# Kernel tuning notes

Hardware: AMD Instinct MI355X
Metric: run time of the kernel (lower is better)

Reference implementation:

```python
import jax, jax.numpy as jnp
import numpy as np

N_NODES = 170000
N_EDGES = 1200000
IN_FEATS = 128
N_HIDDEN = 256
N_CLASSES = 40
BN_EPS = 1e-5


def setup_inputs() -> dict:
    key = jax.random.key(0)
    ks = jax.random.split(key, 12)
    feat = jax.random.normal(ks[0], (N_NODES, IN_FEATS), dtype=jnp.float32)
    src = jax.random.randint(ks[1], (N_EDGES,), 0, N_NODES, dtype=jnp.int32)
    dst = jax.random.randint(ks[2], (N_EDGES,), 0, N_NODES, dtype=jnp.int32)
    # GraphConv weights (glorot-ish scale) and last-layer bias
    W0 = jax.random.normal(ks[3], (IN_FEATS, N_HIDDEN), dtype=jnp.float32) * (1.0 / np.sqrt(IN_FEATS))
    W1 = jax.random.normal(ks[4], (N_HIDDEN, N_HIDDEN), dtype=jnp.float32) * (1.0 / np.sqrt(N_HIDDEN))
    W2 = jax.random.normal(ks[5], (N_HIDDEN, N_CLASSES), dtype=jnp.float32) * (1.0 / np.sqrt(N_HIDDEN))
    b2 = jnp.zeros((N_CLASSES,), dtype=jnp.float32)
    # BatchNorm affine params for the two hidden layers
    g0 = jnp.ones((N_HIDDEN,), dtype=jnp.float32)
    beta0 = jnp.zeros((N_HIDDEN,), dtype=jnp.float32)
    g1 = jnp.ones((N_HIDDEN,), dtype=jnp.float32)
    beta1 = jnp.zeros((N_HIDDEN,), dtype=jnp.float32)
    return {"feat": feat, "src": src, "dst": dst, "W0": W0, "W1": W1, "W2": W2,
            "b2": b2, "g0": g0, "beta0": beta0, "g1": g1, "beta1": beta1}


def _batchnorm(h, gamma, beta):
    mean = jnp.mean(h, axis=0)
    var = jnp.mean((h - mean) ** 2, axis=0)  # biased var, torch training-mode norm
    return (h - mean) * jax.lax.rsqrt(var + BN_EPS) * gamma + beta


def reference(feat, src, dst, W0, W1, W2, b2, g0, beta0, g1, beta1):
    n = feat.shape[0]
    ones_e = jnp.ones(src.shape, dtype=feat.dtype)
    deg_out = jnp.clip(jax.ops.segment_sum(ones_e, src, num_segments=n), 1.0)
    deg_in = jnp.clip(jax.ops.segment_sum(ones_e, dst, num_segments=n), 1.0)
    norm_src = deg_out ** -0.5  # [N]
    norm_dst = deg_in ** -0.5   # [N]

    def conv(h, W, bias=None):
        # GraphConv 'both': D_out^{-1/2} message, sum-aggregate, D_in^{-1/2}
        h = h @ W                              # project first (out <= in)
        msg = h[src] * norm_src[src][:, None]  # [E, out]
        agg = jax.ops.segment_sum(msg, dst, num_segments=n) * norm_dst[:, None]
        if bias is not None:
            agg = agg + bias
        return agg

    # dropout layers are identity in this deterministic (eval-style) reference
    h = conv(feat, W0)
    h = jax.nn.relu(_batchnorm(h, g0, beta0))
    h = conv(h, W1)
    h = jax.nn.relu(_batchnorm(h, g1, beta1))
    h = conv(h, W2, b2)
    return h
```

## Files before the change

kernel.cpp:

```cpp
#include <hip/hip_runtime.h>

#define NN 170000
#define NE 1200000
#define F_IN 128
#define F_HID 256
#define F_OUT 40
#define BN_EPS 1e-5f
#define SCAN_B ((NN + 255) / 256)
#define GB64 ((NN + 63) / 64)
#define STAT_ROWS GB64
#define STAT_CHUNK 32
#define STAT_NCH ((STAT_ROWS + STAT_CHUNK - 1) / STAT_CHUNK)

typedef __attribute__((ext_vector_type(8))) short short8;
typedef __attribute__((ext_vector_type(4))) float f32x4;
typedef __attribute__((ext_vector_type(4))) unsigned short us4;
typedef __attribute__((ext_vector_type(4))) unsigned int u32x4;

__device__ __forceinline__ float b2f(unsigned short u) {
    union { unsigned x; float f; } c; c.x = ((unsigned)u) << 16; return c.f;
}
__device__ __forceinline__ unsigned short f2b(float f) {
    union { float f; unsigned x; } c; c.f = f;
    unsigned r = (c.x + 0x7FFFu + ((c.x >> 16) & 1u)) >> 16;
    return (unsigned short)r;
}

__device__ __forceinline__ void agg_sum(const u32x4& v, float (&aa)[8]) {
    aa[0] += b2f((unsigned short)(v.x & 0xffffu)); aa[1] += b2f((unsigned short)(v.x >> 16));
    aa[2] += b2f((unsigned short)(v.y & 0xffffu)); aa[3] += b2f((unsigned short)(v.y >> 16));
    aa[4] += b2f((unsigned short)(v.z & 0xffffu)); aa[5] += b2f((unsigned short)(v.z >> 16));
    aa[6] += b2f((unsigned short)(v.w & 0xffffu)); aa[7] += b2f((unsigned short)(v.w >> 16));
}
__device__ __forceinline__ void agg_fuse(const u32x4& v, float ns,
        const f32x4& ca0, const f32x4& ca1, const f32x4& cb0, const f32x4& cb1, float (&aa)[8]) {
    aa[0] += fmaxf(fmaf(b2f((unsigned short)(v.x & 0xffffu)), ca0.x, cb0.x), 0.f) * ns;
    aa[1] += fmaxf(fmaf(b2f((unsigned short)(v.x >> 16)),     ca0.y, cb0.y), 0.f) * ns;
    aa[2] += fmaxf(fmaf(b2f((unsigned short)(v.y & 0xffffu)), ca0.z, cb0.z), 0.f) * ns;
    aa[3] += fmaxf(fmaf(b2f((unsigned short)(v.y >> 16)),     ca0.w, cb0.w), 0.f) * ns;
    aa[4] += fmaxf(fmaf(b2f((unsigned short)(v.z & 0xffffu)), ca1.x, cb1.x), 0.f) * ns;
    aa[5] += fmaxf(fmaf(b2f((unsigned short)(v.z >> 16)),     ca1.y, cb1.y), 0.f) * ns;
    aa[6] += fmaxf(fmaf(b2f((unsigned short)(v.w & 0xffffu)), ca1.z, cb1.z), 0.f) * ns;
    aa[7] += fmaxf(fmaf(b2f((unsigned short)(v.w >> 16)),     ca1.w, cb1.w), 0.f) * ns;
}

__global__ void count_kernel(const int* __restrict__ src, const int* __restrict__ dst,
                             int* __restrict__ cnt_src, int* __restrict__ cnt_dst, int E) {
    int e = blockIdx.x * blockDim.x + threadIdx.x;
    if (e < E) {
        atomicAdd(&cnt_src[src[e]], 1);
        atomicAdd(&cnt_dst[dst[e]], 1);
    }
}

__global__ void norm_kernel(const int* __restrict__ cnt_src, const int* __restrict__ cnt_dst,
                            float* __restrict__ norm_src, float* __restrict__ norm_dst, int N) {
    int i = blockIdx.x * blockDim.x + threadIdx.x;
    if (i < N) {
        norm_src[i] = rsqrtf((float)max(cnt_src[i], 1));
        norm_dst[i] = rsqrtf((float)max(cnt_dst[i], 1));
    }
}

__global__ void scan_block_kernel(const int* __restrict__ cnt, int* __restrict__ local,
                                  int* __restrict__ partials, int N) {
    __shared__ int s[256];
    int t = threadIdx.x;
    int idx = blockIdx.x * 256 + t;
    int v = (idx < N) ? cnt[idx] : 0;
    s[t] = v;
    __syncthreads();
    #pragma unroll
    for (int off = 1; off < 256; off <<= 1) {
        int x = (t >= off) ? s[t - off] : 0;
        __syncthreads();
        s[t] += x;
        __syncthreads();
    }
    if (idx < N) local[idx] = s[t] - v;
    if (t == 255) partials[blockIdx.x] = s[t];
}

__global__ void scan_partials_kernel(int* __restrict__ partials, int B) {
    __shared__ int s[1024];
    int t = threadIdx.x;
    int v = (t < B) ? partials[t] : 0;
    s[t] = v;
    __syncthreads();
    #pragma unroll
    for (int off = 1; off < 1024; off <<= 1) {
        int x = (t >= off) ? s[t - off] : 0;
        __syncthreads();
        s[t] += x;
        __syncthreads();
    }
    if (t < B) partials[t] = s[t] - v;
}

__global__ void scan_add_kernel(const int* __restrict__ local, const int* __restrict__ partials,
                                int* __restrict__ row_ptr, int N) {
    int idx = blockIdx.x * blockDim.x + threadIdx.x;
    if (idx < N) row_ptr[idx] = local[idx] + partials[idx >> 8];
    if (idx == 0) row_ptr[N] = NE;
}

__global__ void fill_kernel(const int* __restrict__ src, const int* __restrict__ dst,
                            const int* __restrict__ row_ptr, int* __restrict__ fill,
                            int* __restrict__ csr_src, int E) {
    int e = blockIdx.x * blockDim.x + threadIdx.x;
    if (e < E) {
        int d = dst[e];
        int pos = row_ptr[d] + atomicAdd(&fill[d], 1);
        csr_src[pos] = src[e];
    }
}

__global__ void cast_feat_kernel(const float* __restrict__ feat, const float* __restrict__ norm_src,
                                 unsigned short* __restrict__ featb) {
    unsigned idx = blockIdx.x * blockDim.x + threadIdx.x;
    if (idx >= (unsigned)NN * (F_IN / 4)) return;
    float ns = norm_src[idx / (F_IN / 4)];
    f32x4 v = __builtin_nontemporal_load((const f32x4*)(feat + (size_t)idx * 4));
    us4 o; o.x = f2b(v.x * ns); o.y = f2b(v.y * ns); o.z = f2b(v.z * ns); o.w = f2b(v.w * ns);
    *(us4*)(featb + (size_t)idx * 4) = o;
}

template<int K, int M, int MP>
__global__ void wt_kernel(const float* __restrict__ W, unsigned short* __restrict__ Wt) {
    int idx = blockIdx.x * blockDim.x + threadIdx.x;
    if (idx >= MP * K) return;
    int m = idx / K, k = idx % K;
    float v = (m < M) ? W[(size_t)k * M + m] : 0.0f;
    Wt[idx] = f2b(v);
}

__global__ void stat_reduce_kernel(const float* __restrict__ part, float* __restrict__ red) {
    int c = threadIdx.x;
    int ch = blockIdx.x;
    int r0 = ch * STAT_CHUNK;
    int r1 = min(r0 + STAT_CHUNK, STAT_ROWS);
    float s = 0.f;
    for (int r = r0; r < r1; r++) s += part[(size_t)r * 512 + c];
    red[ch * 512 + c] = s;
}

__global__ void bn_finalize2_kernel(const float* __restrict__ red,
                                    const float* __restrict__ gamma, const float* __restrict__ beta,
                                    float* __restrict__ a, float* __restrict__ b) {
    int c = threadIdx.x;
    float sum = 0.f, sumsq = 0.f;
    for (int ch = 0; ch < STAT_NCH; ch++) {
        sum   += red[ch * 512 + c];
        sumsq += red[ch * 512 + 256 + c];
    }
    float invN = 1.0f / (float)NN;
    float mean = sum * invN;
    float var = sumsq * invN - mean * mean;
    float inv = rsqrtf(var + BN_EPS);
    float ac = inv * gamma[c];
    a[c] = ac;
    b[c] = beta[c] - mean * ac;
}

template<int F, int WM_T, int WN_T, int WAVES_N, bool FUSE, bool LAST>
__global__ __launch_bounds__(256) void fused_gather_gemm(
        const unsigned short* __restrict__ h,
        const int* __restrict__ row_ptr, const int* __restrict__ csr_src,
        const float* __restrict__ bna, const float* __restrict__ bnb,
        const unsigned short* __restrict__ Wt,
        const float* __restrict__ norm_src, const float* __restrict__ norm_dst,
        const float* __restrict__ bias,
        void* __restrict__ C, float* __restrict__ opart, int N) {
    constexpr int BM = 64;
    constexpr int LPN = F / 8;
    constexpr int NPW = 64 / LPN;
    constexpr int WAVES_M = 4 / WAVES_N;
    __shared__ unsigned short As[BM * F];

    const int lane = threadIdx.x & 63;
    const int wave = threadIdx.x >> 6;
    const int r0 = blockIdx.x * BM;

    {
        const int sub = lane / LPN;
        const int cl = lane % LPN;
        f32x4 ca0 = {0,0,0,0}, ca1 = {0,0,0,0}, cb0 = {0,0,0,0}, cb1 = {0,0,0,0};
        if (FUSE) {
            ca0 = *(const f32x4*)(bna + cl * 8);
            ca1 = *(const f32x4*)(bna + cl * 8 + 4);
            cb0 = *(const f32x4*)(bnb + cl * 8);
            cb1 = *(const f32x4*)(bnb + cl * 8 + 4);
        }
        #pragma unroll
        for (int g = 0; g < 16 / NPW; g++) {
            int nl = wave * 16 + g * NPW + sub;
            int node = r0 + nl;
            float aa[8] = {0.f, 0.f, 0.f, 0.f, 0.f, 0.f, 0.f, 0.f};
            int beg = 0, end = 0;
            if (node < N) { beg = row_ptr[node]; end = row_ptr[node + 1]; }
            int e = beg;
            for (; e + 2 <= end; e += 2) {
                int s0 = csr_src[e], s1 = csr_src[e + 1];
                u32x4 v0 = *(const u32x4*)(h + (size_t)s0 * F + cl * 8);
                u32x4 v1 = *(const u32x4*)(h + (size_t)s1 * F + cl * 8);
                if (FUSE) {
                    agg_fuse(v0, norm_src[s0], ca0, ca1, cb0, cb1, aa);
                    agg_fuse(v1, norm_src[s1], ca0, ca1, cb0, cb1, aa);
                } else {
                    agg_sum(v0, aa); agg_sum(v1, aa);
                }
            }
            if (e < end) {
                int s0 = csr_src[e];
                u32x4 v0 = *(const u32x4*)(h + (size_t)s0 * F + cl * 8);
                if (FUSE) agg_fuse(v0, norm_src[s0], ca0, ca1, cb0, cb1, aa);
                else      agg_sum(v0, aa);
            }
            u32x4 d;
            d.x = (unsigned)f2b(aa[0]) | ((unsigned)f2b(aa[1]) << 16);
            d.y = (unsigned)f2b(aa[2]) | ((unsigned)f2b(aa[3]) << 16);
            d.z = (unsigned)f2b(aa[4]) | ((unsigned)f2b(aa[5]) << 16);
            d.w = (unsigned)f2b(aa[6]) | ((unsigned)f2b(aa[7]) << 16);
            unsigned off = ((unsigned)(nl * (F * 2) + cl * 16)) ^ (((unsigned)nl & 7u) << 4);
            *(u32x4*)((char*)As + off) = d;
        }
    }
    __syncthreads();

    const int quad = lane >> 4, l15 = lane & 15;
    const int wr = wave / WAVES_N, wc = wave % WAVES_N;
    const int wmb = wr * WM_T * 16;
    const int wnb = wc * WN_T * 16;

    const unsigned short* bptr[WN_T];
    #pragma unroll
    for (int j = 0; j < WN_T; j++)
        bptr[j] = Wt + (size_t)(wnb + j * 16 + l15) * F + quad * 8;

    f32x4 acc[WM_T][WN_T] = {};
    #pragma unroll
    for (int kk = 0; kk < F; kk += 32) {
        short8 af[WM_T], bf[WN_T];
        #pragma unroll
        for (int i = 0; i < WM_T; i++) {
            int row = wmb + i * 16 + l15;
            unsigned off = ((unsigned)(row * (F * 2) + (kk + quad * 8) * 2)) ^ (((unsigned)row & 7u) << 4);
            af[i] = *(const short8*)((const char*)As + off);
        }
        #pragma unroll
        for (int j = 0; j < WN_T; j++)
            bf[j] = *(const short8*)(bptr[j] + kk);
        #pragma unroll
        for (int i = 0; i < WM_T; i++)
            #pragma unroll
            for (int j = 0; j < WN_T; j++)
                acc[i][j] = __builtin_amdgcn_mfma_f32_16x16x32_bf16(af[i], bf[j], acc[i][j], 0, 0, 0);
    }

    float s[WN_T] = {}, ss[WN_T] = {};
    #pragma unroll
    for (int i = 0; i < WM_T; i++) {
        #pragma unroll
        for (int r = 0; r < 4; r++) {
            int row = r0 + wmb + i * 16 + quad * 4 + r;
            if (row >= N) continue;
            float nd = norm_dst[row];
            #pragma unroll
            for (int j = 0; j < WN_T; j++) {
                float v = acc[i][j][r] * nd;
                int col = wnb + j * 16 + l15;
                if (LAST) {
                    if (col < F_OUT)
                        ((float*)C)[(size_t)row * F_OUT + col] = v + bias[col];
                } else {
                    s[j] += v; ss[j] += v * v;
                    ((unsigned short*)C)[(size_t)row * F_HID + col] = f2b(v);
                }
            }
        }
    }
    if (!LAST) {
        #pragma unroll
        for (int j = 0; j < WN_T; j++) {
            float t = s[j], t2 = ss[j];
            t  += __shfl_xor(t, 16);  t  += __shfl_xor(t, 32);
            t2 += __shfl_xor(t2, 16); t2 += __shfl_xor(t2, 32);
            if (quad == 0) {
                int col = wnb + j * 16 + l15;
                size_t prow = (size_t)(blockIdx.x * WAVES_M + wr) * 512;
                opart[prow + col] = t;
                opart[prow + 256 + col] = t2;
            }
        }
    }
}

extern "C" void kernel_launch(void* const* d_in, const int* in_sizes, int n_in,
                              void* d_out, int out_size, void* d_ws, size_t ws_size,
                              hipStream_t stream) {
    const float* feat  = (const float*)d_in[0];
    const int*   src   = (const int*)d_in[1];
    const int*   dst   = (const int*)d_in[2];
    const float* W0    = (const float*)d_in[3];
    const float* W1    = (const float*)d_in[4];
    const float* W2    = (const float*)d_in[5];
    const float* b2    = (const float*)d_in[6];
    const float* g0    = (const float*)d_in[7];
    const float* beta0 = (const float*)d_in[8];
    const float* g1    = (const float*)d_in[9];
    const float* beta1 = (const float*)d_in[10];
    float* out = (float*)d_out;

    const int N = NN, E = NE;

    char* ws = (char*)d_ws;
    auto alloc_b = [&](size_t bytes) {
        void* p = (void*)ws;
        ws += ((bytes + 255) / 256) * 256;
        return p;
    };
    float* norm_src = (float*)alloc_b((size_t)N * 4);
    float* norm_dst = (float*)alloc_b((size_t)N * 4);
    int*   row_ptr  = (int*)alloc_b((size_t)(N + 1) * 4);
    int*   csr_src  = (int*)alloc_b((size_t)E * 4);
    float* bnpart   = (float*)alloc_b((size_t)STAT_ROWS * 512 * 4);
    float* bnred    = (float*)alloc_b((size_t)STAT_NCH * 512 * 4);
    float* bn_a0    = (float*)alloc_b(256 * 4);
    float* bn_b0    = (float*)alloc_b(256 * 4);
    float* bn_a1    = (float*)alloc_b(256 * 4);
    float* bn_b1    = (float*)alloc_b(256 * 4);
    unsigned short* Wt0 = (unsigned short*)alloc_b((size_t)256 * 128 * 2);
    unsigned short* Wt1 = (unsigned short*)alloc_b((size_t)256 * 256 * 2);
    unsigned short* Wt2 = (unsigned short*)alloc_b((size_t)64 * 256 * 2);
    void* B1 = alloc_b((size_t)N * 512);
    void* B2 = alloc_b((size_t)N * 512);
    unsigned short* featb = (unsigned short*)alloc_b((size_t)N * F_IN * 2);

    unsigned short* B1b = (unsigned short*)B1;
    unsigned short* B2b = (unsigned short*)B2;

    int* cnt_src  = (int*)B1;
    int* cnt_dst  = cnt_src + N;
    int* fill     = cnt_dst + N;
    int* local    = fill + N;
    int* partials = local + N;

    hipMemsetAsync(cnt_src, 0, ((size_t)4 * N + 1024) * 4, stream);
    count_kernel<<<(E + 255) / 256, 256, 0, stream>>>(src, dst, cnt_src, cnt_dst, E);
    norm_kernel<<<(N + 255) / 256, 256, 0, stream>>>(cnt_src, cnt_dst, norm_src, norm_dst, N);
    scan_block_kernel<<<SCAN_B, 256, 0, stream>>>(cnt_dst, local, partials, N);
    scan_partials_kernel<<<1, 1024, 0, stream>>>(partials, SCAN_B);
    scan_add_kernel<<<(N + 255) / 256, 256, 0, stream>>>(local, partials, row_ptr, N);
    fill_kernel<<<(E + 255) / 256, 256, 0, stream>>>(src, dst, row_ptr, fill, csr_src, E);
    wt_kernel<128, 256, 256><<<(256 * 128 + 255) / 256, 256, 0, stream>>>(W0, Wt0);
    wt_kernel<256, 256, 256><<<(256 * 256 + 255) / 256, 256, 0, stream>>>(W1, Wt1);
    wt_kernel<256, 40, 64><<<(64 * 256 + 255) / 256, 256, 0, stream>>>(W2, Wt2);
    cast_feat_kernel<<<((unsigned)N * (F_IN / 4) + 255) / 256, 256, 0, stream>>>(feat, norm_src, featb);

    fused_gather_gemm<128, 4, 4, 4, false, false><<<GB64, 256, 0, stream>>>(
        featb, row_ptr, csr_src, nullptr, nullptr, Wt0, nullptr, norm_dst, nullptr, B1, bnpart, N);
    stat_reduce_kernel<<<STAT_NCH, 512, 0, stream>>>(bnpart, bnred);
    bn_finalize2_kernel<<<1, 256, 0, stream>>>(bnred, g0, beta0, bn_a0, bn_b0);

    fused_gather_gemm<256, 4, 4, 4, true, false><<<GB64, 256, 0, stream>>>(
        B1b, row_ptr, csr_src, bn_a0, bn_b0, Wt1, norm_src, norm_dst, nullptr, B2, bnpart, N);
    stat_reduce_kernel<<<STAT_NCH, 512, 0, stream>>>(bnpart, bnred);
    bn_finalize2_kernel<<<1, 256, 0, stream>>>(bnred, g1, beta1, bn_a1, bn_b1);

    fused_gather_gemm<256, 1, 3, 1, true, true><<<GB64, 256, 0, stream>>>(
        B2b, row_ptr, csr_src, bn_a1, bn_b1, Wt2, norm_src, norm_dst, b2, out, nullptr, N);
}
```

Measured before the change: 819.9 us.

## Reorder last layer to project before gather and unroll edge loop by four

```diff
diff --git a/kernel.cpp b/kernel.cpp
--- a/kernel.cpp
+++ b/kernel.cpp
@@ -8,6 +8,7 @@
 #define BN_EPS 1e-5f
 #define SCAN_B ((NN + 255) / 256)
 #define GB64 ((NN + 63) / 64)
+#define GB128 ((NN + 127) / 128)
 #define STAT_ROWS GB64
 #define STAT_CHUNK 32
 #define STAT_NCH ((STAT_ROWS + STAT_CHUNK - 1) / STAT_CHUNK)
@@ -24,6 +25,13 @@
     union { float f; unsigned x; } c; c.f = f;
     unsigned r = (c.x + 0x7FFFu + ((c.x >> 16) & 1u)) >> 16;
     return (unsigned short)r;
+}
+__device__ __forceinline__ unsigned bn2(unsigned u, float a0, float b0, float a1, float b1) {
+    float lo = b2f((unsigned short)(u & 0xffffu));
+    float hi = b2f((unsigned short)(u >> 16));
+    lo = fmaxf(lo * a0 + b0, 0.0f);
+    hi = fmaxf(hi * a1 + b1, 0.0f);
+    return (unsigned)f2b(lo) | ((unsigned)f2b(hi) << 16);
 }
 
 __device__ __forceinline__ void agg_sum(const u32x4& v, float (&aa)[8]) {
@@ -199,13 +207,33 @@
             int beg = 0, end = 0;
             if (node < N) { beg = row_ptr[node]; end = row_ptr[node + 1]; }
             int e = beg;
+            for (; e + 4 <= end; e += 4) {
+                int s0 = csr_src[e],     s1 = csr_src[e + 1];
+                int s2 = csr_src[e + 2], s3 = csr_src[e + 3];
+                u32x4 v0 = *(const u32x4*)(h + (size_t)s0 * F + cl * 8);
+                u32x4 v1 = *(const u32x4*)(h + (size_t)s1 * F + cl * 8);
+                u32x4 v2 = *(const u32x4*)(h + (size_t)s2 * F + cl * 8);
+                u32x4 v3 = *(const u32x4*)(h + (size_t)s3 * F + cl * 8);
+                if (FUSE) {
+                    float n0 = norm_src[s0], n1 = norm_src[s1];
+                    float n2 = norm_src[s2], n3 = norm_src[s3];
+                    agg_fuse(v0, n0, ca0, ca1, cb0, cb1, aa);
+                    agg_fuse(v1, n1, ca0, ca1, cb0, cb1, aa);
+                    agg_fuse(v2, n2, ca0, ca1, cb0, cb1, aa);
+                    agg_fuse(v3, n3, ca0, ca1, cb0, cb1, aa);
+                } else {
+                    agg_sum(v0, aa); agg_sum(v1, aa);
+                    agg_sum(v2, aa); agg_sum(v3, aa);
+                }
+            }
             for (; e + 2 <= end; e += 2) {
                 int s0 = csr_src[e], s1 = csr_src[e + 1];
                 u32x4 v0 = *(const u32x4*)(h + (size_t)s0 * F + cl * 8);
                 u32x4 v1 = *(const u32x4*)(h + (size_t)s1 * F + cl * 8);
                 if (FUSE) {
-                    agg_fuse(v0, norm_src[s0], ca0, ca1, cb0, cb1, aa);
-                    agg_fuse(v1, norm_src[s1], ca0, ca1, cb0, cb1, aa);
+                    float n0 = norm_src[s0], n1 = norm_src[s1];
+                    agg_fuse(v0, n0, ca0, ca1, cb0, cb1, aa);
+                    agg_fuse(v1, n1, ca0, ca1, cb0, cb1, aa);
                 } else {
                     agg_sum(v0, aa); agg_sum(v1, aa);
                 }
@@ -293,6 +321,109 @@
             }
         }
     }
+}
+
+__global__ __launch_bounds__(256, 3) void gemm2_kernel(const unsigned short* __restrict__ A,
+                                                       const unsigned short* __restrict__ Wt,
+                                                       const float* __restrict__ norm_src,
+                                                       const float* __restrict__ bna,
+                                                       const float* __restrict__ bnb,
+                                                       float* __restrict__ C, int N) {
+    constexpr int K = 256, WM_T = 2, WN_T = 4;
+    const int lane = threadIdx.x & 63;
+    const int wave = threadIdx.x >> 6;
+    const int quad = lane >> 4, l15 = lane & 15;
+    const int r0 = blockIdx.x * 128;
+    const int wmb = wave * WM_T * 16;
+
+    const unsigned short* aptr[WM_T];
+    #pragma unroll
+    for (int i = 0; i < WM_T; i++) {
+        int gr = r0 + wmb + i * 16 + l15;
+        if (gr > N - 1) gr = N - 1;
+        aptr[i] = A + (size_t)gr * K + quad * 8;
+    }
+    const unsigned short* bptr[WN_T];
+    #pragma unroll
+    for (int j = 0; j < WN_T; j++)
+        bptr[j] = Wt + (size_t)(j * 16 + l15) * K + quad * 8;
+
+    f32x4 acc[WM_T][WN_T] = {};
+    #pragma unroll
+    for (int kk = 0; kk < K; kk += 32) {
+        int kb = kk + quad * 8;
+        const f32x4 a0 = *(const f32x4*)(bna + kb);
+        const f32x4 a1 = *(const f32x4*)(bna + kb + 4);
+        const f32x4 s0 = *(const f32x4*)(bnb + kb);
+        const f32x4 s1 = *(const f32x4*)(bnb + kb + 4);
+        short8 af[WM_T], bf[WN_T];
+        #pragma unroll
+        for (int i = 0; i < WM_T; i++) {
+            u32x4 u = *(const u32x4*)(aptr[i] + kk);
+            u.x = bn2(u.x, a0.x, s0.x, a0.y, s0.y);
+            u.y = bn2(u.y, a0.z, s0.z, a0.w, s0.w);
+            u.z = bn2(u.z, a1.x, s1.x, a1.y, s1.y);
+            u.w = bn2(u.w, a1.z, s1.z, a1.w, s1.w);
+            af[i] = *(short8*)&u;
+        }
+        #pragma unroll
+        for (int j = 0; j < WN_T; j++)
+            bf[j] = *(const short8*)(bptr[j] + kk);
+        #pragma unroll
+        for (int i = 0; i < WM_T; i++)
+            #pragma unroll
+            for (int j = 0; j < WN_T; j++)
+                acc[i][j] = __builtin_amdgcn_mfma_f32_16x16x32_bf16(af[i], bf[j], acc[i][j], 0, 0, 0);
+    }
+
+    #pragma unroll
+    for (int i = 0; i < WM_T; i++) {
+        #pragma unroll
+        for (int r = 0; r < 4; r++) {
+            int row = r0 + wmb + i * 16 + quad * 4 + r;
+            if (row >= N) continue;
+            float ns = norm_src[row];
+            #pragma unroll
+            for (int j = 0; j < WN_T; j++) {
+                int col = j * 16 + l15;
+                if (col < F_OUT)
+                    C[(size_t)row * F_OUT + col] = acc[i][j][r] * ns;
+            }
+        }
+    }
+}
+
+__global__ void gather_final_kernel(const float* __restrict__ h, const int* __restrict__ row_ptr,
+                                    const int* __restrict__ csr_src,
+                                    const float* __restrict__ norm_dst, const float* __restrict__ bias,
+                                    float* __restrict__ out, int N) {
+    constexpr int TPN = F_OUT / 4;
+    unsigned idx = blockIdx.x * blockDim.x + threadIdx.x;
+    if (idx >= (unsigned)N * TPN) return;
+    unsigned node = idx / TPN;
+    unsigned g = idx % TPN;
+    int beg = row_ptr[node], end = row_ptr[node + 1];
+    float ax0 = 0.f, ay0 = 0.f, az0 = 0.f, aw0 = 0.f;
+    float ax1 = 0.f, ay1 = 0.f, az1 = 0.f, aw1 = 0.f;
+    int e = beg;
+    for (; e + 2 <= end; e += 2) {
+        int s0 = csr_src[e], s1 = csr_src[e + 1];
+        const f32x4 v0 = *(const f32x4*)(h + (size_t)s0 * F_OUT + g * 4);
+        const f32x4 v1 = *(const f32x4*)(h + (size_t)s1 * F_OUT + g * 4);
+        ax0 += v0.x; ay0 += v0.y; az0 += v0.z; aw0 += v0.w;
+        ax1 += v1.x; ay1 += v1.y; az1 += v1.z; aw1 += v1.w;
+    }
+    if (e < end) {
+        int s0 = csr_src[e];
+        const f32x4 v0 = *(const f32x4*)(h + (size_t)s0 * F_OUT + g * 4);
+        ax0 += v0.x; ay0 += v0.y; az0 += v0.z; aw0 += v0.w;
+    }
+    float nd = norm_dst[node];
+    const f32x4 b = *(const f32x4*)(bias + g * 4);
+    f32x4 r;
+    r.x = (ax0 + ax1) * nd + b.x; r.y = (ay0 + ay1) * nd + b.y;
+    r.z = (az0 + az1) * nd + b.z; r.w = (aw0 + aw1) * nd + b.w;
+    __builtin_nontemporal_store(r, (f32x4*)(out + (size_t)node * F_OUT + g * 4));
 }
 
 extern "C" void kernel_launch(void* const* d_in, const int* in_sizes, int n_in,
@@ -338,6 +469,7 @@
 
     unsigned short* B1b = (unsigned short*)B1;
     unsigned short* B2b = (unsigned short*)B2;
+    float*          B1f = (float*)B1;
 
     int* cnt_src  = (int*)B1;
     int* cnt_dst  = cnt_src + N;
@@ -367,6 +499,10 @@
     stat_reduce_kernel<<<STAT_NCH, 512, 0, stream>>>(bnpart, bnred);
     bn_finalize2_kernel<<<1, 256, 0, stream>>>(bnred, g1, beta1, bn_a1, bn_b1);
 
-    fused_gather_gemm<256, 1, 3, 1, true, true><<<GB64, 256, 0, stream>>>(
-        B2b, row_ptr, csr_src, bn_a1, bn_b1, Wt2, norm_src, norm_dst, b2, out, nullptr, N);
-}
+    gemm2_kernel<<<GB128, 256, 0, stream>>>(B2b, Wt2, norm_src, bn_a1, bn_b1, B1f, N);
+    {
+        unsigned total = (unsigned)N * (F_OUT / 4);
+        gather_final_kernel<<<(total + 255) / 256, 256, 0, stream>>>(
+            B1f, row_ptr, csr_src, norm_dst, b2, out, N);
+    }
+}
```

Result: faster. 764.6 us (-6.7%).
